# Kernel tuning notes

Hardware: AMD Instinct MI355X
Metric: run time of the kernel (lower is better)

## Reference

```python
import jax, jax.numpy as jnp
import numpy as np

K = 1024
H = 128

def setup_inputs() -> dict:
    key = jax.random.key(0)
    ks = jax.random.split(key, 11)
    s = lambda fan_in: 1.0 / np.sqrt(fan_in)
    # coord_mlp: Linear(H, H//2) -> GELU -> Linear(H//2, 2)
    cW1 = jax.random.uniform(ks[0], (H, H // 2), minval=-s(H), maxval=s(H))
    cb1 = jax.random.uniform(ks[1], (H // 2,), minval=-s(H), maxval=s(H))
    cW2 = jax.random.uniform(ks[2], (H // 2, 2), minval=-s(H // 2), maxval=s(H // 2))
    cb2 = jax.random.uniform(ks[3], (2,), minval=-s(H // 2), maxval=s(H // 2))
    # edge_mlp: Linear(2H, H) -> GELU -> Linear(H, H//2) -> GELU -> Linear(H//2, 1)
    eW1 = jax.random.uniform(ks[4], (2 * H, H), minval=-s(2 * H), maxval=s(2 * H))
    eb1 = jax.random.uniform(ks[5], (H,), minval=-s(2 * H), maxval=s(2 * H))
    eW2 = jax.random.uniform(ks[6], (H, H // 2), minval=-s(H), maxval=s(H))
    eb2 = jax.random.uniform(ks[7], (H // 2,), minval=-s(H), maxval=s(H))
    eW3 = jax.random.uniform(ks[8], (H // 2, 1), minval=-s(H // 2), maxval=s(H // 2))
    eb3 = jax.random.uniform(ks[9], (1,), minval=-s(H // 2), maxval=s(H // 2))
    z_s = jax.random.normal(ks[10], (K, H), dtype=jnp.float32)
    return {"z_s": z_s, "cW1": cW1, "cb1": cb1, "cW2": cW2, "cb2": cb2,
            "eW1": eW1, "eb1": eb1, "eW2": eW2, "eb2": eb2, "eW3": eW3, "eb3": eb3}

def reference(z_s, cW1, cb1, cW2, cb2, eW1, eb1, eW2, eb2, eW3, eb3):
    gelu = lambda x: jax.nn.gelu(x, approximate=False)  # torch default GELU is exact erf form
    # coords: [k, 2]
    coords_pred = gelu(z_s @ cW1 + cb1) @ cW2 + cb2
    # edge first layer: cat([zi, zj]) @ eW1 == zi @ eW1[:H] + zj @ eW1[H:]
    # (same math as the broadcast-concat, without materializing [k, k, 2H])
    pi = z_s @ eW1[:H]   # [k, H]
    pj = z_s @ eW1[H:]   # [k, H]
    h1 = gelu(pi[:, None, :] + pj[None, :, :] + eb1)   # [k, k, H]
    h2 = gelu(h1 @ eW2 + eb2)                          # [k, k, H//2]
    adj_logits = (h2 @ eW3 + eb3)[..., 0]              # [k, k]
    adj_logits = (adj_logits + adj_logits.T) / 2.0
    return (coords_pred, adj_logits)
```

## Files before the change

kernel.cpp:

```cpp
#include <hip/hip_runtime.h>
#include <hip/hip_fp16.h>


#define KN 1024
#define HN 128

typedef float  floatx4 __attribute__((ext_vector_type(4)));
typedef _Float16 half8v __attribute__((ext_vector_type(8)));

__device__ __forceinline__ float gelu_f(float x) {
    float x2 = x * x;
    float t  = fmaf(x2, -0.1029434f, -2.3022087f);
    float e  = __builtin_amdgcn_exp2f(x * t);
    return x * __builtin_amdgcn_rcpf(e + 1.0f);
}

__device__ __forceinline__ unsigned int gelu2u(unsigned int xu) {
    __half2 x  = __builtin_bit_cast(__half2, xu);
    __half2 x2 = __hmul2(x, x);
    __half2 t  = __hfma2(x2, __float2half2_rn(-0.1029434f),
                             __float2half2_rn(-2.3022087f));
    __half2 e  = h2exp2(__hmul2(x, t));
    __half2 r  = h2rcp(__hadd2(e, __float2half2_rn(1.0f)));
    return __builtin_bit_cast(unsigned int, __hmul2(x, r));
}

__device__ __forceinline__ unsigned int cvt2u(float a, float b) {
    return __builtin_bit_cast(unsigned int, __builtin_amdgcn_cvt_pkrtz(a, b));
}

__device__ __forceinline__ float dotw3(const floatx4* acc, half8v w3f0,
                                       half8v w3f1, float b3) {
    uint4 u0, u1;
    u0.x = gelu2u(cvt2u(acc[0][0], acc[0][1]));
    u0.y = gelu2u(cvt2u(acc[0][2], acc[0][3]));
    u0.z = gelu2u(cvt2u(acc[1][0], acc[1][1]));
    u0.w = gelu2u(cvt2u(acc[1][2], acc[1][3]));
    u1.x = gelu2u(cvt2u(acc[2][0], acc[2][1]));
    u1.y = gelu2u(cvt2u(acc[2][2], acc[2][3]));
    u1.z = gelu2u(cvt2u(acc[3][0], acc[3][1]));
    u1.w = gelu2u(cvt2u(acc[3][2], acc[3][3]));
    half8v h20 = __builtin_bit_cast(half8v, u0);
    half8v h21 = __builtin_bit_cast(half8v, u1);
    floatx4 d = (floatx4){b3, b3, b3, b3};
    d = __builtin_amdgcn_mfma_f32_16x16x32_f16(w3f0, h20, d, 0, 0, 0);
    d = __builtin_amdgcn_mfma_f32_16x16x32_f16(w3f1, h21, d, 0, 0, 0);
    return d[0];
}

__global__ __launch_bounds__(256) void prep_kernel(
    const float* __restrict__ z,   const float* __restrict__ cW1,
    const float* __restrict__ cb1, const float* __restrict__ cW2,
    const float* __restrict__ cb2, const float* __restrict__ eW1,
    const float* __restrict__ eb1, const float* __restrict__ eW2,
    const float* __restrict__ eW3,
    _Float16* __restrict__ pi_h,   _Float16* __restrict__ pj_h,
    _Float16* __restrict__ w2T,    _Float16* __restrict__ w3h,
    float* __restrict__ coords ) {
    __shared__ float z8[8][128];
    __shared__ float c1s[8][64];
    const int tid = threadIdx.x;
    const int r0  = blockIdx.x * 8;

    if (blockIdx.x < 32) {
        int e = blockIdx.x * 256 + tid;
        int d = e >> 7, k = e & 127;
        int R = ((d >> 5) & 1) * 32 + ((d >> 2) & 1) * 16 +
                ((d >> 3) & 3) * 4  + (d & 3);
        w2T[R * 128 + k] = (_Float16)eW2[k * 64 + d];
    }
    if (blockIdx.x == 32 && tid < 64) w3h[tid] = (_Float16)eW3[tid];

#pragma unroll
    for (int s = 0; s < 4; ++s) {
        int e = tid + 256 * s;
        z8[e >> 7][e & 127] = z[r0 * HN + e];
    }
    __syncthreads();

    const int col = tid & 127, which = tid >> 7;
    const float* w = eW1 + which * HN * HN + col;
    float acc8[8] = {0.f, 0.f, 0.f, 0.f, 0.f, 0.f, 0.f, 0.f};
    for (int k = 0; k < HN; ++k) {
        float wv = w[k * HN];
#pragma unroll
        for (int r = 0; r < 8; ++r) acc8[r] = fmaf(z8[r][k], wv, acc8[r]);
    }
    if (which == 0) {
        float b = eb1[col];
#pragma unroll
        for (int r = 0; r < 8; ++r)
            pi_h[(r0 + r) * HN + col] = (_Float16)(acc8[r] + b);
    } else {
#pragma unroll
        for (int r = 0; r < 8; ++r)
            pj_h[(r0 + r) * HN + col] = (_Float16)acc8[r];
    }

#pragma unroll
    for (int s = 0; s < 2; ++s) {
        int task = tid + 256 * s;
        int row = task >> 6, mid = task & 63;
        float a = cb1[mid];
        for (int k = 0; k < HN; ++k) a = fmaf(z8[row][k], cW1[k * 64 + mid], a);
        c1s[row][mid] = gelu_f(a);
    }
    __syncthreads();
    if (tid < 16) {
        int row = tid >> 1, o = tid & 1;
        float a = cb2[o];
#pragma unroll 8
        for (int m = 0; m < 64; ++m) a = fmaf(c1s[row][m], cW2[m * 2 + o], a);
        coords[(r0 + row) * 2 + o] = a;
    }
}

__global__ __launch_bounds__(512, 4) void edge_kernel(
    const _Float16* __restrict__ pi_h, const _Float16* __restrict__ pj_h,
    const _Float16* __restrict__ w2T,  const _Float16* __restrict__ w3h,
    const float* __restrict__ eb2,     const float* __restrict__ eb3,
    float* __restrict__ out_adj) {
    __shared__ __align__(16) unsigned int w2_s[64 * 64];
    const int i0 = blockIdx.y * 32, j0 = blockIdx.x * 32;
    const int tid = threadIdx.x;

    const unsigned int* piu = (const unsigned int*)pi_h;
    const unsigned int* pju = (const unsigned int*)pj_h;
    const unsigned int* w2u = (const unsigned int*)w2T;

#pragma unroll
    for (int s = 0; s < 2; ++s) {
        int e = tid * 4 + 2048 * s;
        int r = e >> 6;
        uint4 v = *reinterpret_cast<const uint4*>(&w2u[e]);
        *reinterpret_cast<uint4*>(&w2_s[e ^ ((r & 7) << 2)]) = v;
    }

    const int lane = tid & 63;
    const int wave = tid >> 6;
    const int lrow = lane & 15;
    const int lhi  = lane >> 4;
    const int lhi4 = lhi << 2;
    const int lhi8 = lhi << 3;
    const int swzW = (lrow & 7) << 2;

    const unsigned int* pjA = &pju[(j0 + lrow) * 64];
    const unsigned int* pjB = &pju[(j0 + 16 + lrow) * 64];
    half8v bA[4], bB[4];
#pragma unroll
    for (int q = 0; q < 4; ++q) {
        const int ko = (q << 4) | lhi4;
        bA[q] = *reinterpret_cast<const half8v*>(&pjA[ko]);
        bB[q] = *reinterpret_cast<const half8v*>(&pjB[ko]);
    }
    const unsigned int* w2base = &w2_s[lrow << 6];

    const half8v w3f0 = *reinterpret_cast<const half8v*>(&w3h[lhi8]);
    const half8v w3f1 = *reinterpret_cast<const half8v*>(&w3h[32 + lhi8]);
    const float4 e0 = *reinterpret_cast<const float4*>(&eb2[lhi8]);
    const float4 e1 = *reinterpret_cast<const float4*>(&eb2[lhi8 + 4]);
    const float4 e2 = *reinterpret_cast<const float4*>(&eb2[32 + lhi8]);
    const float4 e3 = *reinterpret_cast<const float4*>(&eb2[36 + lhi8]);
    const float b3 = eb3[0];
    __syncthreads();

#pragma unroll
    for (int t = 0; t < 4; ++t) {
        const int iL = (wave << 2) + t;
        const unsigned int* pirow = &piu[(size_t)(i0 + iL) * 64];

        floatx4 accA[4], accB[4];
        accA[0] = (floatx4){e0.x, e0.y, e0.z, e0.w};
        accA[1] = (floatx4){e1.x, e1.y, e1.z, e1.w};
        accA[2] = (floatx4){e2.x, e2.y, e2.z, e2.w};
        accA[3] = (floatx4){e3.x, e3.y, e3.z, e3.w};
#pragma unroll
        for (int c = 0; c < 4; ++c) accB[c] = accA[c];

#pragma unroll
        for (int q = 0; q < 4; ++q) {
            const int ko = (q << 4) | lhi4;
            half8v a = *reinterpret_cast<const half8v*>(&pirow[ko]);

            uint4 sA = __builtin_bit_cast(uint4, a + bA[q]);
            uint4 gA;
            gA.x = gelu2u(sA.x); gA.y = gelu2u(sA.y);
            gA.z = gelu2u(sA.z); gA.w = gelu2u(sA.w);
            half8v afA = __builtin_bit_cast(half8v, gA);

            uint4 sB = __builtin_bit_cast(uint4, a + bB[q]);
            uint4 gB;
            gB.x = gelu2u(sB.x); gB.y = gelu2u(sB.y);
            gB.z = gelu2u(sB.z); gB.w = gelu2u(sB.w);
            half8v afB = __builtin_bit_cast(half8v, gB);

            const int kw = ko ^ swzW;
#pragma unroll
            for (int c = 0; c < 4; ++c) {
                half8v bf = *reinterpret_cast<const half8v*>(
                    &w2base[(c << 10) + kw]);
                accA[c] = __builtin_amdgcn_mfma_f32_16x16x32_f16(
                    bf, afA, accA[c], 0, 0, 0);
                accB[c] = __builtin_amdgcn_mfma_f32_16x16x32_f16(
                    bf, afB, accB[c], 0, 0, 0);
            }
        }

        const float dA = dotw3(accA, w3f0, w3f1, b3);
        const float dB = dotw3(accB, w3f0, w3f1, b3);
        if (lhi == 0) {
            float* row = &out_adj[(size_t)(i0 + iL) * KN + j0];
            row[lrow]      = dA;
            row[16 + lrow] = dB;
        }
    }
}

__global__ __launch_bounds__(256) void sym_kernel(float* __restrict__ adj) {
    int idx = blockIdx.x * 256 + threadIdx.x;
    int i = idx >> 10, j = idx & 1023;
    if (j < i) return;
    float a = adj[i * KN + j];
    float b = adj[j * KN + i];
    float m = 0.5f * (a + b);
    adj[i * KN + j] = m;
    adj[j * KN + i] = m;
}

extern "C" void kernel_launch(void* const* d_in, const int* in_sizes, int n_in,
                              void* d_out, int out_size, void* d_ws, size_t ws_size,
                              hipStream_t stream) {
    const float* z   = (const float*)d_in[0];
    const float* cW1 = (const float*)d_in[1];
    const float* cb1 = (const float*)d_in[2];
    const float* cW2 = (const float*)d_in[3];
    const float* cb2 = (const float*)d_in[4];
    const float* eW1 = (const float*)d_in[5];
    const float* eb1 = (const float*)d_in[6];
    const float* eW2 = (const float*)d_in[7];
    const float* eb2 = (const float*)d_in[8];
    const float* eW3 = (const float*)d_in[9];
    const float* eb3 = (const float*)d_in[10];

    float* out = (float*)d_out;
    _Float16* pi_h = (_Float16*)d_ws;
    _Float16* pj_h = pi_h + KN * HN;
    _Float16* w2T  = pj_h + KN * HN;
    _Float16* w3h  = w2T + 64 * HN;

    prep_kernel<<<128, 256, 0, stream>>>(z, cW1, cb1, cW2, cb2, eW1, eb1, eW2,
                                         eW3, pi_h, pj_h, w2T, w3h, out);

    dim3 gridB(32, 32);
    edge_kernel<<<gridB, 512, 0, stream>>>(pi_h, pj_h, w2T, w3h, eb2, eb3,
                                           out + 2048);

    sym_kernel<<<4096, 256, 0, stream>>>(out + 2048);
}
```

Baseline: 81.43 us.

## Fuse symmetrization into edge kernel over upper-triangular block pairs

The edge kernel now launches one block per upper-triangular 32x32 tile pair (528 blocks). Each block computes both the (i,j) and (j,i) tiles, holds the first in shared memory, averages them and writes both symmetric outputs, so the separate sym_kernel launch and its read-modify-write pass over the adjacency matrix go away. The prep kernel is also split into 4-row blocks (256 blocks) to use more CUs. The same MLP work is still done, but diagonal blocks compute their tile twice, and the grid is smaller, so the GPU may fill less evenly.

```diff
diff --git a/kernel.cpp b/kernel.cpp
--- a/kernel.cpp
+++ b/kernel.cpp
@@ -57,10 +57,10 @@
     _Float16* __restrict__ pi_h,   _Float16* __restrict__ pj_h,
     _Float16* __restrict__ w2T,    _Float16* __restrict__ w3h,
     float* __restrict__ coords ) {
-    __shared__ float z8[8][128];
-    __shared__ float c1s[8][64];
+    __shared__ float z4[4][128];
+    __shared__ float c1s[4][64];
     const int tid = threadIdx.x;
-    const int r0  = blockIdx.x * 8;
+    const int r0  = blockIdx.x * 4;
 
     if (blockIdx.x < 32) {
         int e = blockIdx.x * 256 + tid;
@@ -72,41 +72,39 @@
     if (blockIdx.x == 32 && tid < 64) w3h[tid] = (_Float16)eW3[tid];
 
 #pragma unroll
-    for (int s = 0; s < 4; ++s) {
+    for (int s = 0; s < 2; ++s) {
         int e = tid + 256 * s;
-        z8[e >> 7][e & 127] = z[r0 * HN + e];
+        z4[e >> 7][e & 127] = z[r0 * HN + e];
     }
     __syncthreads();
 
     const int col = tid & 127, which = tid >> 7;
     const float* w = eW1 + which * HN * HN + col;
-    float acc8[8] = {0.f, 0.f, 0.f, 0.f, 0.f, 0.f, 0.f, 0.f};
+    float acc4[4] = {0.f, 0.f, 0.f, 0.f};
     for (int k = 0; k < HN; ++k) {
         float wv = w[k * HN];
 #pragma unroll
-        for (int r = 0; r < 8; ++r) acc8[r] = fmaf(z8[r][k], wv, acc8[r]);
+        for (int r = 0; r < 4; ++r) acc4[r] = fmaf(z4[r][k], wv, acc4[r]);
     }
     if (which == 0) {
         float b = eb1[col];
 #pragma unroll
-        for (int r = 0; r < 8; ++r)
-            pi_h[(r0 + r) * HN + col] = (_Float16)(acc8[r] + b);
+        for (int r = 0; r < 4; ++r)
+            pi_h[(r0 + r) * HN + col] = (_Float16)(acc4[r] + b);
     } else {
 #pragma unroll
-        for (int r = 0; r < 8; ++r)
-            pj_h[(r0 + r) * HN + col] = (_Float16)acc8[r];
-    }
-
-#pragma unroll
-    for (int s = 0; s < 2; ++s) {
-        int task = tid + 256 * s;
-        int row = task >> 6, mid = task & 63;
+        for (int r = 0; r < 4; ++r)
+            pj_h[(r0 + r) * HN + col] = (_Float16)acc4[r];
+    }
+
+    {
+        int row = tid >> 6, mid = tid & 63;
         float a = cb1[mid];
-        for (int k = 0; k < HN; ++k) a = fmaf(z8[row][k], cW1[k * 64 + mid], a);
+        for (int k = 0; k < HN; ++k) a = fmaf(z4[row][k], cW1[k * 64 + mid], a);
         c1s[row][mid] = gelu_f(a);
     }
     __syncthreads();
-    if (tid < 16) {
+    if (tid < 8) {
         int row = tid >> 1, o = tid & 1;
         float a = cb2[o];
 #pragma unroll 8
@@ -121,8 +119,15 @@
     const float* __restrict__ eb2,     const float* __restrict__ eb3,
     float* __restrict__ out_adj) {
     __shared__ __align__(16) unsigned int w2_s[64 * 64];
-    const int i0 = blockIdx.y * 32, j0 = blockIdx.x * 32;
+    __shared__ float tb[32][33];
     const int tid = threadIdx.x;
+
+    int b = blockIdx.x;
+    int bi = (int)((sqrtf(8.0f * (float)b + 1.0f) - 1.0f) * 0.5f);
+    while ((bi + 1) * (bi + 2) / 2 <= b) ++bi;
+    while (bi * (bi + 1) / 2 > b) --bi;
+    const int bj = b - bi * (bi + 1) / 2;
+    const int i0 = bi * 32, j0 = bj * 32;
 
     const unsigned int* piu = (const unsigned int*)pi_h;
     const unsigned int* pju = (const unsigned int*)pj_h;
@@ -143,16 +148,6 @@
     const int lhi4 = lhi << 2;
     const int lhi8 = lhi << 3;
     const int swzW = (lrow & 7) << 2;
-
-    const unsigned int* pjA = &pju[(j0 + lrow) * 64];
-    const unsigned int* pjB = &pju[(j0 + 16 + lrow) * 64];
-    half8v bA[4], bB[4];
-#pragma unroll
-    for (int q = 0; q < 4; ++q) {
-        const int ko = (q << 4) | lhi4;
-        bA[q] = *reinterpret_cast<const half8v*>(&pjA[ko]);
-        bB[q] = *reinterpret_cast<const half8v*>(&pjB[ko]);
-    }
     const unsigned int* w2base = &w2_s[lrow << 6];
 
     const half8v w3f0 = *reinterpret_cast<const half8v*>(&w3h[lhi8]);
@@ -164,67 +159,80 @@
     const float b3 = eb3[0];
     __syncthreads();
 
-#pragma unroll
-    for (int t = 0; t < 4; ++t) {
-        const int iL = (wave << 2) + t;
-        const unsigned int* pirow = &piu[(size_t)(i0 + iL) * 64];
-
-        floatx4 accA[4], accB[4];
-        accA[0] = (floatx4){e0.x, e0.y, e0.z, e0.w};
-        accA[1] = (floatx4){e1.x, e1.y, e1.z, e1.w};
-        accA[2] = (floatx4){e2.x, e2.y, e2.z, e2.w};
-        accA[3] = (floatx4){e3.x, e3.y, e3.z, e3.w};
-#pragma unroll
-        for (int c = 0; c < 4; ++c) accB[c] = accA[c];
-
+    for (int pass = 0; pass < 2; ++pass) {
+        const int rb = pass ? i0 : j0;
+        const int cb = pass ? j0 : i0;
+
+        const unsigned int* pjA = &pju[(cb + lrow) * 64];
+        const unsigned int* pjB = &pju[(cb + 16 + lrow) * 64];
+        half8v bA[4], bB[4];
 #pragma unroll
         for (int q = 0; q < 4; ++q) {
             const int ko = (q << 4) | lhi4;
-            half8v a = *reinterpret_cast<const half8v*>(&pirow[ko]);
-
-            uint4 sA = __builtin_bit_cast(uint4, a + bA[q]);
-            uint4 gA;
-            gA.x = gelu2u(sA.x); gA.y = gelu2u(sA.y);
-            gA.z = gelu2u(sA.z); gA.w = gelu2u(sA.w);
-            half8v afA = __builtin_bit_cast(half8v, gA);
-
-            uint4 sB = __builtin_bit_cast(uint4, a + bB[q]);
-            uint4 gB;
-            gB.x = gelu2u(sB.x); gB.y = gelu2u(sB.y);
-            gB.z = gelu2u(sB.z); gB.w = gelu2u(sB.w);
-            half8v afB = __builtin_bit_cast(half8v, gB);
-
-            const int kw = ko ^ swzW;
-#pragma unroll
-            for (int c = 0; c < 4; ++c) {
-                half8v bf = *reinterpret_cast<const half8v*>(
-                    &w2base[(c << 10) + kw]);
-                accA[c] = __builtin_amdgcn_mfma_f32_16x16x32_f16(
-                    bf, afA, accA[c], 0, 0, 0);
-                accB[c] = __builtin_amdgcn_mfma_f32_16x16x32_f16(
-                    bf, afB, accB[c], 0, 0, 0);
+            bA[q] = *reinterpret_cast<const half8v*>(&pjA[ko]);
+            bB[q] = *reinterpret_cast<const half8v*>(&pjB[ko]);
+        }
+
+#pragma unroll
+        for (int t = 0; t < 4; ++t) {
+            const int iL = (wave << 2) + t;
+            const unsigned int* pirow = &piu[(size_t)(rb + iL) * 64];
+
+            floatx4 accA[4], accB[4];
+            accA[0] = (floatx4){e0.x, e0.y, e0.z, e0.w};
+            accA[1] = (floatx4){e1.x, e1.y, e1.z, e1.w};
+            accA[2] = (floatx4){e2.x, e2.y, e2.z, e2.w};
+            accA[3] = (floatx4){e3.x, e3.y, e3.z, e3.w};
+#pragma unroll
+            for (int c = 0; c < 4; ++c) accB[c] = accA[c];
+
+#pragma unroll
+            for (int q = 0; q < 4; ++q) {
+                const int ko = (q << 4) | lhi4;
+                half8v a = *reinterpret_cast<const half8v*>(&pirow[ko]);
+
+                uint4 sA = __builtin_bit_cast(uint4, a + bA[q]);
+                uint4 gA;
+                gA.x = gelu2u(sA.x); gA.y = gelu2u(sA.y);
+                gA.z = gelu2u(sA.z); gA.w = gelu2u(sA.w);
+                half8v afA = __builtin_bit_cast(half8v, gA);
+
+                uint4 sB = __builtin_bit_cast(uint4, a + bB[q]);
+                uint4 gB;
+                gB.x = gelu2u(sB.x); gB.y = gelu2u(sB.y);
+                gB.z = gelu2u(sB.z); gB.w = gelu2u(sB.w);
+                half8v afB = __builtin_bit_cast(half8v, gB);
+
+                const int kw = ko ^ swzW;
+#pragma unroll
+                for (int c = 0; c < 4; ++c) {
+                    half8v bf = *reinterpret_cast<const half8v*>(
+                        &w2base[(c << 10) + kw]);
+                    accA[c] = __builtin_amdgcn_mfma_f32_16x16x32_f16(
+                        bf, afA, accA[c], 0, 0, 0);
+                    accB[c] = __builtin_amdgcn_mfma_f32_16x16x32_f16(
+                        bf, afB, accB[c], 0, 0, 0);
+                }
+            }
+
+            const float dA = dotw3(accA, w3f0, w3f1, b3);
+            const float dB = dotw3(accB, w3f0, w3f1, b3);
+            if (lhi == 0) {
+                if (pass == 0) {
+                    tb[iL][lrow]      = dA;
+                    tb[iL][16 + lrow] = dB;
+                } else {
+                    float a1 = 0.5f * (dA + tb[lrow][iL]);
+                    float a2 = 0.5f * (dB + tb[16 + lrow][iL]);
+                    out_adj[(size_t)(i0 + iL) * KN + j0 + lrow]      = a1;
+                    out_adj[(size_t)(j0 + lrow) * KN + i0 + iL]      = a1;
+                    out_adj[(size_t)(i0 + iL) * KN + j0 + 16 + lrow] = a2;
+                    out_adj[(size_t)(j0 + 16 + lrow) * KN + i0 + iL] = a2;
+                }
             }
         }
-
-        const float dA = dotw3(accA, w3f0, w3f1, b3);
-        const float dB = dotw3(accB, w3f0, w3f1, b3);
-        if (lhi == 0) {
-            float* row = &out_adj[(size_t)(i0 + iL) * KN + j0];
-            row[lrow]      = dA;
-            row[16 + lrow] = dB;
-        }
-    }
-}
-
-__global__ __launch_bounds__(256) void sym_kernel(float* __restrict__ adj) {
-    int idx = blockIdx.x * 256 + threadIdx.x;
-    int i = idx >> 10, j = idx & 1023;
-    if (j < i) return;
-    float a = adj[i * KN + j];
-    float b = adj[j * KN + i];
-    float m = 0.5f * (a + b);
-    adj[i * KN + j] = m;
-    adj[j * KN + i] = m;
+        if (pass == 0) __syncthreads();
+    }
 }
 
 extern "C" void kernel_launch(void* const* d_in, const int* in_sizes, int n_in,
@@ -248,12 +256,9 @@
     _Float16* w2T  = pj_h + KN * HN;
     _Float16* w3h  = w2T + 64 * HN;
 
-    prep_kernel<<<128, 256, 0, stream>>>(z, cW1, cb1, cW2, cb2, eW1, eb1, eW2,
+    prep_kernel<<<256, 256, 0, stream>>>(z, cW1, cb1, cW2, cb2, eW1, eb1, eW2,
                                          eW3, pi_h, pj_h, w2T, w3h, out);
 
-    dim3 gridB(32, 32);
-    edge_kernel<<<gridB, 512, 0, stream>>>(pi_h, pj_h, w2T, w3h, eb2, eb3,
-                                           out + 2048);
-
-    sym_kernel<<<4096, 256, 0, stream>>>(out + 2048);
-}
+    edge_kernel<<<528, 512, 0, stream>>>(pi_h, pj_h, w2T, w3h, eb2, eb3,
+                                         out + 2048);
+}
```

Measured after the change: 102.3 us. +25.7%, slower.
